# Kernel tuning notes

Hardware: AMD Instinct MI355X
Metric: run time of the kernel (lower is better)

Reference implementation:

```python
import jax, jax.numpy as jnp
import numpy as np

B, T, C = 2, 2048, 2048
H = 16
ROPE_DIM, NOPE_DIM, V_DIM = 64, 64, 128
HEAD_DIM = NOPE_DIM + ROPE_DIM  # 128
Q_RANK, KV_RANK = 1536, 512


def setup_inputs() -> dict:
    key = jax.random.key(0)
    ks = jax.random.split(key, 8)
    std = 0.02
    return {
        "x": jax.random.normal(ks[0], (B, T, C), jnp.float32),
        "cos": jax.random.normal(ks[1], (1, T, 1, ROPE_DIM // 2), jnp.float32),
        "sin": jax.random.normal(ks[2], (1, T, 1, ROPE_DIM // 2), jnp.float32),
        "wq_down": jax.random.normal(ks[3], (Q_RANK, C), jnp.float32) * std,
        "wq_up": jax.random.normal(ks[4], (H * HEAD_DIM, Q_RANK), jnp.float32) * std,
        "wkv_down": jax.random.normal(ks[5], (KV_RANK, C), jnp.float32) * std,
        "wkv_up": jax.random.normal(ks[6], (H * (HEAD_DIM + V_DIM), KV_RANK), jnp.float32) * std,
        "wo": jax.random.normal(ks[7], (C, H * V_DIM), jnp.float32) * std,
    }


def _rope(x, cos, sin):
    # x: [B, T, H, rope_dim]
    d = x.shape[-1] // 2
    x1, x2 = x[..., :d], x[..., d:]
    return jnp.concatenate([x1 * cos + x2 * sin, -x1 * sin + x2 * cos], axis=-1)


def _rms_norm(x):
    eps = jnp.finfo(x.dtype).eps
    return x * jax.lax.rsqrt(jnp.mean(jnp.square(x), axis=-1, keepdims=True) + eps)


def reference(x, cos, sin, wq_down, wq_up, wkv_down, wkv_up, wo):
    # Low-rank q projection
    q = jnp.einsum('btc,rc,dr->btd', x, wq_down, wq_up)
    q = q.reshape(B, T, H, HEAD_DIM)
    q_nope, q_rope = q[..., :NOPE_DIM], q[..., NOPE_DIM:]
    # Low-rank kv projection (naive decompression)
    kv = jnp.einsum('btc,rc,dr->btd', x, wkv_down, wkv_up)
    kv = kv.reshape(B, T, H, HEAD_DIM + V_DIM)
    k_nope = kv[..., :NOPE_DIM]
    k_rope = kv[..., NOPE_DIM:HEAD_DIM]
    v = kv[..., HEAD_DIM:]
    # Partial RoPE on the rope sub-dims only
    q_rope = _rope(q_rope, cos, sin)
    k_rope = _rope(k_rope, cos, sin)
    q = _rms_norm(jnp.concatenate([q_nope, q_rope], axis=-1))
    k = _rms_norm(jnp.concatenate([k_nope, k_rope], axis=-1))
    # Causal SDPA: [B, H, T, T]
    scale = 1.0 / jnp.sqrt(jnp.float32(HEAD_DIM))
    scores = jnp.einsum('bthd,bshd->bhts', q, k) * scale
    causal = jnp.tril(jnp.ones((T, T), dtype=bool))
    scores = jnp.where(causal, scores, jnp.finfo(scores.dtype).min)
    probs = jax.nn.softmax(scores, axis=-1)
    y = jnp.einsum('bhts,bshd->bthd', probs, v).reshape(B, T, H * V_DIM)
    return y @ wo.T
```

## Files before the change

### kernel.cpp

```cpp
#include <hip/hip_runtime.h>
#include <hip/hip_bf16.h>
#include <math.h>
#include <type_traits>

#define AS1 __attribute__((address_space(1)))
#define AS3 __attribute__((address_space(3)))

typedef __bf16  bf16x8 __attribute__((ext_vector_type(8)));
typedef float   f32x4  __attribute__((ext_vector_type(4)));
typedef float   f32x16 __attribute__((ext_vector_type(16)));
typedef __hip_bfloat16 bf16;

#define MFMA16x16x32 __builtin_amdgcn_mfma_f32_16x16x32_bf16
#define MFMA32x32x16 __builtin_amdgcn_mfma_f32_32x32x16_bf16

__device__ __forceinline__ void gload16(const void* g, void* l) {
  __builtin_amdgcn_global_load_lds((const AS1 void*)g, (AS3 void*)l, 16, 0, 0);
}

__device__ __forceinline__ unsigned short bfbits(float v) {
  return __builtin_bit_cast(unsigned short, __float2bfloat16(v));
}

struct CastArgs {
  const float4* src[6];
  ushort4* dst[6];
  unsigned bound[6];
};

__global__ __launch_bounds__(256) void f2bf_multi(CastArgs a) {
  unsigned i = blockIdx.x * 256 + threadIdx.x;
  if (i >= a.bound[5]) return;
  unsigned lo = 0;
  int s = 0;
#pragma unroll
  for (int k = 0; k < 5; k++) {
    if (i >= a.bound[k]) { s = k + 1; lo = a.bound[k]; }
  }
  unsigned idx = i - lo;
  float4 v = a.src[s][idx];
  ushort4 o;
  o.x = bfbits(v.x); o.y = bfbits(v.y); o.z = bfbits(v.z); o.w = bfbits(v.w);
  a.dst[s][idx] = o;
}

template <typename OutT>
__global__ __launch_bounds__(256, 3) void gemm_bt(const bf16* __restrict__ A,
                                                  const bf16* __restrict__ W,
                                                  OutT* __restrict__ Cp,
                                                  int M, int N, int K, int lda) {
  __shared__ __align__(16) bf16 As[128 * 32];
  __shared__ __align__(16) bf16 Ws[128 * 32];
  const int t = threadIdx.x;
  const int w = t >> 6, lane = t & 63;
  const int quad = lane >> 4, l16 = lane & 15;
  const int wr = (w >> 1) * 64, wc = (w & 1) * 64;
  const size_t m0 = (size_t)blockIdx.x * 128;
  const size_t n0 = (size_t)blockIdx.y * 128;
  const int rowS = t >> 2;
  const int kch  = (t & 3) * 8;

  f32x4 acc[4][4];
#pragma unroll
  for (int i = 0; i < 4; i++)
#pragma unroll
    for (int j = 0; j < 4; j++) acc[i][j] = f32x4{0.f, 0.f, 0.f, 0.f};

  for (int k0 = 0; k0 < K; k0 += 32) {
    __syncthreads();
    gload16(A + (m0 + rowS) * (size_t)lda + k0 + kch,      (char*)As + w * 1024);
    gload16(A + (m0 + rowS + 64) * (size_t)lda + k0 + kch, (char*)As + 4096 + w * 1024);
    gload16(W + (n0 + rowS) * (size_t)K + k0 + kch,        (char*)Ws + w * 1024);
    gload16(W + (n0 + rowS + 64) * (size_t)K + k0 + kch,   (char*)Ws + 4096 + w * 1024);
    __syncthreads();

    bf16x8 af[4], bw[4];
#pragma unroll
    for (int i = 0; i < 4; i++)
      af[i] = *(const bf16x8*)(As + (wr + i * 16 + l16) * 32 + quad * 8);
#pragma unroll
    for (int j = 0; j < 4; j++)
      bw[j] = *(const bf16x8*)(Ws + (wc + j * 16 + l16) * 32 + quad * 8);
#pragma unroll
    for (int i = 0; i < 4; i++)
#pragma unroll
      for (int j = 0; j < 4; j++)
        acc[i][j] = MFMA16x16x32(af[i], bw[j], acc[i][j], 0, 0, 0);
  }

#pragma unroll
  for (int i = 0; i < 4; i++)
#pragma unroll
    for (int j = 0; j < 4; j++)
#pragma unroll
      for (int r = 0; r < 4; r++) {
        size_t row = m0 + wr + i * 16 + quad * 4 + r;
        size_t col = n0 + wc + j * 16 + l16;
        float v = acc[i][j][r];
        if constexpr (std::is_same<OutT, float>::value)
          Cp[row * N + col] = v;
        else
          Cp[row * N + col] = __float2bfloat16(v);
      }
}

__global__ __launch_bounds__(256, 3) void gemm_kvup(const bf16* __restrict__ A,
                                                    const bf16* __restrict__ W,
                                                    bf16* __restrict__ kvraw,
                                                    bf16* __restrict__ vT) {
  __shared__ __align__(16) bf16 As[128 * 32];
  __shared__ __align__(16) bf16 Ws[128 * 32];
  const int t = threadIdx.x;
  const int w = t >> 6, lane = t & 63;
  const int quad = lane >> 4, l16 = lane & 15;
  const int wr = (w >> 1) * 64, wc = (w & 1) * 64;
  const size_t m0 = (size_t)blockIdx.x * 128;
  const int n0 = (int)blockIdx.y * 128;
  const int rowS = t >> 2;
  const int kch  = (t & 3) * 8;
  const int K = 512, lda = 2048;

  f32x4 acc[4][4];
#pragma unroll
  for (int i = 0; i < 4; i++)
#pragma unroll
    for (int j = 0; j < 4; j++) acc[i][j] = f32x4{0.f, 0.f, 0.f, 0.f};

  for (int k0 = 0; k0 < K; k0 += 32) {
    __syncthreads();
    gload16(A + (m0 + rowS) * (size_t)lda + k0 + kch,        (char*)As + w * 1024);
    gload16(A + (m0 + rowS + 64) * (size_t)lda + k0 + kch,   (char*)As + 4096 + w * 1024);
    gload16(W + ((size_t)n0 + rowS) * K + k0 + kch,          (char*)Ws + w * 1024);
    gload16(W + ((size_t)n0 + rowS + 64) * K + k0 + kch,     (char*)Ws + 4096 + w * 1024);
    __syncthreads();

    bf16x8 af[4], bw[4];
#pragma unroll
    for (int i = 0; i < 4; i++)
      af[i] = *(const bf16x8*)(As + (wr + i * 16 + l16) * 32 + quad * 8);
#pragma unroll
    for (int j = 0; j < 4; j++)
      bw[j] = *(const bf16x8*)(Ws + (wc + j * 16 + l16) * 32 + quad * 8);
#pragma unroll
    for (int i = 0; i < 4; i++)
#pragma unroll
      for (int j = 0; j < 4; j++)
        acc[i][j] = MFMA16x16x32(af[i], bw[j], acc[i][j], 0, 0, 0);
  }

  if ((n0 & 128) == 0) {
#pragma unroll
    for (int i = 0; i < 4; i++)
#pragma unroll
      for (int j = 0; j < 4; j++)
#pragma unroll
        for (int r = 0; r < 4; r++) {
          size_t row = m0 + wr + i * 16 + quad * 4 + r;
          size_t col = (size_t)n0 + wc + j * 16 + l16;
          kvraw[row * 4096 + col] = __float2bfloat16(acc[i][j][r]);
        }
  } else {
    const int h = n0 >> 8;
#pragma unroll
    for (int i = 0; i < 4; i++) {
      size_t row = m0 + wr + i * 16 + quad * 4;
      int bb = (int)(row >> 11), tloc = (int)(row & 2047);
#pragma unroll
      for (int j = 0; j < 4; j++) {
        int d = wc + j * 16 + l16;
        ushort4 v4;
        v4.x = bfbits(acc[i][j][0]);
        v4.y = bfbits(acc[i][j][1]);
        v4.z = bfbits(acc[i][j][2]);
        v4.w = bfbits(acc[i][j][3]);
        *(ushort4*)(vT + ((size_t)(bb * 16 + h) * 128 + d) * 2048 + tloc) = v4;
      }
    }
  }
}

__global__ __launch_bounds__(256) void rope_rms(const bf16* __restrict__ qraw,
                                                const bf16* __restrict__ kvraw,
                                                const float* __restrict__ cosp,
                                                const float* __restrict__ sinp,
                                                bf16* __restrict__ qn,
                                                bf16* __restrict__ kn) {
  const int bt = blockIdx.x;
  const int w = threadIdx.x >> 6, lane = threadIdx.x & 63;
  const int h = blockIdx.y * 4 + w;
  const int tt = bt & 2047;
  const float c = cosp[tt * 32 + (lane & 31)];
  const float s = sinp[tt * 32 + (lane & 31)];
  const float inv128 = 1.0f / 128.0f;
  const float eps = 1.1920929e-7f;

  {
    const bf16* base = qraw + (size_t)bt * 2048 + h * 128;
    float a = (float)base[lane];
    float o = (float)base[64 + lane];
    float partner = __shfl_xor(o, 32);
    float orope = (lane < 32) ? (o * c + partner * s) : (o * c - partner * s);
    float ss = a * a + orope * orope;
#pragma unroll
    for (int off = 1; off < 64; off <<= 1) ss += __shfl_xor(ss, off);
    float rn = rsqrtf(ss * inv128 + eps);
    bf16* outp = qn + ((size_t)bt * 16 + h) * 128;
    outp[lane] = __float2bfloat16(a * rn);
    outp[64 + lane] = __float2bfloat16(orope * rn);
  }
  {
    const bf16* base = kvraw + (size_t)bt * 4096 + h * 256;
    float a = (float)base[lane];
    float o = (float)base[64 + lane];
    float partner = __shfl_xor(o, 32);
    float orope = (lane < 32) ? (o * c + partner * s) : (o * c - partner * s);
    float ss = a * a + orope * orope;
#pragma unroll
    for (int off = 1; off < 64; off <<= 1) ss += __shfl_xor(ss, off);
    float rn = rsqrtf(ss * inv128 + eps);
    bf16* outp = kn + ((size_t)bt * 16 + h) * 128;
    outp[lane] = __float2bfloat16(a * rn);
    outp[64 + lane] = __float2bfloat16(orope * rn);
  }
}

__global__ __launch_bounds__(128, 2) void attn_kernel(const bf16* __restrict__ qn,
                                                      const bf16* __restrict__ kn,
                                                      const bf16* __restrict__ vT,
                                                      bf16* __restrict__ y) {
  __shared__ __align__(16) bf16 Ks[64 * 128];
  __shared__ __align__(16) bf16 Vs[128 * 64];
  __shared__ __align__(16) bf16 Ps[2][32 * 64];
  const int t = threadIdx.x, w = t >> 6, lane = t & 63;
  const int l32 = lane & 31, hl = lane >> 5;
  const int b = blockIdx.x >> 4, h = blockIdx.x & 15;
  const int yy = (int)blockIdx.y;
  const int y0 = yy & 7, k4 = yy >> 3;
  int xb;
  if (k4 == 0) xb = 31 - y0;
  else if (k4 == 1) xb = y0;
  else if (k4 == 2) xb = 23 - y0;
  else xb = 8 + y0;
  const int q0 = xb * 64;
  const int T_ = 2048, H_ = 16;

  bf16x8 qf[8];
  {
    const bf16* qbase = qn + ((size_t)(b * T_ + q0 + w * 32 + l32) * H_ + h) * 128;
#pragma unroll
    for (int ki = 0; ki < 8; ki++)
      qf[ki] = *(const bf16x8*)(qbase + ki * 16 + hl * 8);
  }

  f32x16 yacc[4];
#pragma unroll
  for (int db = 0; db < 4; db++)
#pragma unroll
    for (int i = 0; i < 16; i++) yacc[db][i] = 0.f;
  float lrow[16];
#pragma unroll
  for (int r = 0; r < 16; r++) lrow[r] = 0.f;
  const float K1 = 0.08838834764831845f * 1.4426950408889634f;
  const float K2 = -12.0f * 1.4426950408889634f;
  const int ntiles = xb + 1;

  for (int it = 0; it < ntiles; ++it) {
    const int s0 = it * 64;
    __syncthreads();
#pragma unroll
    for (int is = 0; is < 8; ++is) {
      int i = is * 2 + w;
      int srow = i * 4 + (lane >> 4);
      int cg = (lane & 15) ^ (srow & 7);
      gload16(kn + ((size_t)(b * T_ + s0 + srow) * H_ + h) * 128 + cg * 8,
              (char*)Ks + i * 1024);
    }
#pragma unroll
    for (int is = 0; is < 8; ++is) {
      int i = is * 2 + w;
      int drow = i * 8 + (lane >> 3);
      int cg = (lane & 7) ^ (drow & 7);
      gload16(vT + ((size_t)(b * H_ + h) * 128 + drow) * T_ + s0 + cg * 8,
              (char*)Vs + i * 1024);
    }
    __syncthreads();

    f32x16 sacc[2];
#pragma unroll
    for (int cb = 0; cb < 2; cb++)
#pragma unroll
      for (int i = 0; i < 16; i++) sacc[cb][i] = 0.f;
#pragma unroll
    for (int cb = 0; cb < 2; ++cb) {
      const int s = cb * 32 + l32;
#pragma unroll
      for (int ki = 0; ki < 8; ++ki) {
        int pos = (ki * 2 + hl) ^ (s & 7);
        bf16x8 kf = *(const bf16x8*)(Ks + s * 128 + pos * 8);
        sacc[cb] = MFMA32x32x16(qf[ki], kf, sacc[cb], 0, 0, 0);
      }
    }

    const bool diag = (it == xb);
#pragma unroll
    for (int cb = 0; cb < 2; ++cb) {
      const int sidx = cb * 32 + l32;
      const int sg = s0 + sidx;
#pragma unroll
      for (int r = 0; r < 16; ++r) {
        const int row = (r & 3) + 8 * (r >> 2) + 4 * hl;
        float e;
        if (diag && (sg > q0 + w * 32 + row))
          e = 0.0f;
        else
          e = exp2f(fmaf(sacc[cb][r], K1, K2));
        lrow[r] += e;
        Ps[w][row * 64 + (((sidx >> 3) ^ (row & 7)) << 3) + (sidx & 7)] =
            __float2bfloat16(e);
      }
    }
    __asm__ volatile("s_waitcnt lgkmcnt(0)" ::: "memory");

#pragma unroll
    for (int ki = 0; ki < 4; ++ki) {
      int ppos = (ki * 2 + hl) ^ (l32 & 7);
      bf16x8 pf = *(const bf16x8*)(&Ps[w][l32 * 64 + ppos * 8]);
#pragma unroll
      for (int db = 0; db < 4; ++db) {
        int d = db * 32 + l32;
        int vpos = (ki * 2 + hl) ^ (d & 7);
        bf16x8 vf = *(const bf16x8*)(Vs + d * 64 + vpos * 8);
        yacc[db] = MFMA32x32x16(pf, vf, yacc[db], 0, 0, 0);
      }
    }
  }

#pragma unroll
  for (int r = 0; r < 16; r++) {
#pragma unroll
    for (int off = 1; off < 32; off <<= 1) lrow[r] += __shfl_xor(lrow[r], off);
  }
#pragma unroll
  for (int r = 0; r < 16; r++) {
    const int row = (r & 3) + 8 * (r >> 2) + 4 * hl;
    float inv = 1.0f / lrow[r];
    size_t qrow = (size_t)(b * T_ + q0 + w * 32 + row);
    bf16* outp = y + qrow * 2048 + h * 128;
#pragma unroll
    for (int db = 0; db < 4; db++)
      outp[db * 32 + l32] = __float2bfloat16(yacc[db][r] * inv);
  }
}

extern "C" void kernel_launch(void* const* d_in, const int* in_sizes, int n_in,
                              void* d_out, int out_size, void* d_ws, size_t ws_size,
                              hipStream_t stream) {
  (void)in_sizes; (void)n_in; (void)out_size; (void)ws_size;
  const float* x    = (const float*)d_in[0];
  const float* cosp = (const float*)d_in[1];
  const float* sinp = (const float*)d_in[2];
  const float* wqd  = (const float*)d_in[3];
  const float* wqu  = (const float*)d_in[4];
  const float* wkvd = (const float*)d_in[5];
  const float* wkvu = (const float*)d_in[6];
  const float* wo   = (const float*)d_in[7];
  float* out = (float*)d_out;

  char* ws = (char*)d_ws;
  size_t off = 0;
  auto alloc = [&](size_t elems) { bf16* p = (bf16*)(ws + off); off += elems * 2; return p; };
  bf16* xb      = alloc((size_t)4096 * 2048);
  bf16* wqdB    = alloc((size_t)1536 * 2048);
  bf16* wkvdB   = alloc((size_t)512 * 2048);
  bf16* wquB    = alloc((size_t)2048 * 1536);
  bf16* wkvuB   = alloc((size_t)4096 * 512);
  bf16* woB     = alloc((size_t)2048 * 2048);
  bf16* qkvdown = alloc((size_t)4096 * 2048);
  bf16* qraw    = alloc((size_t)4096 * 2048);
  bf16* kvraw   = alloc((size_t)4096 * 4096);
  bf16* qnb     = alloc((size_t)4096 * 16 * 128);
  bf16* knb     = alloc((size_t)4096 * 16 * 128);
  bf16* vTb     = alloc((size_t)2 * 16 * 128 * 2048);
  bf16* yb      = alloc((size_t)4096 * 2048);

  CastArgs ca;
  const float* srcs[6] = {x, wqd, wkvd, wqu, wkvu, wo};
  bf16* dsts[6]        = {xb, wqdB, wkvdB, wquB, wkvuB, woB};
  size_t cnts[6] = {(size_t)4096 * 2048, (size_t)1536 * 2048, (size_t)512 * 2048,
                    (size_t)2048 * 1536, (size_t)4096 * 512,  (size_t)2048 * 2048};
  unsigned cum = 0;
  for (int i = 0; i < 6; i++) {
    ca.src[i] = (const float4*)srcs[i];
    ca.dst[i] = (ushort4*)dsts[i];
    cum += (unsigned)(cnts[i] / 4);
    ca.bound[i] = cum;
  }
  f2bf_multi<<<dim3((cum + 255) / 256), 256, 0, stream>>>(ca);

  gemm_bt<bf16><<<dim3(32, 16), 256, 0, stream>>>(xb, wqdB, qkvdown, 4096, 2048, 2048, 2048);
  gemm_bt<bf16><<<dim3(32, 16), 256, 0, stream>>>(qkvdown, wquB, qraw, 4096, 2048, 1536, 2048);
  gemm_kvup<<<dim3(32, 32), 256, 0, stream>>>(qkvdown + 1536, wkvuB, kvraw, vTb);
  rope_rms<<<dim3(4096, 4), 256, 0, stream>>>(qraw, kvraw, cosp, sinp, qnb, knb);
  attn_kernel<<<dim3(32, 32), 128, 0, stream>>>(qnb, knb, vTb, yb);
  gemm_bt<float><<<dim3(32, 16), 256, 0, stream>>>(yb, woB, out, 4096, 2048, 2048, 2048);
}
```

Measured before the change: 393.8 us.

## Split attention block into four 16-row waves using 16x16x32 MFMA

The attention kernel now runs each 64-query block with four wavefronts of 16 rows each, instead of two wavefronts of 32 rows. It switches from 32x32x16 to 16x16x32 MFMA and reorganises the Q, score, P and output fragment layouts to match. K/V tile loads are now spread over four waves, and each thread holds fewer registers. The goal is more waves per CU, better latency hiding and less load per wave, at the cost of a lower MFMA tile size and more LDS traffic per FLOP, since V fragments are reread per 16-row wave.

```diff
diff --git a/kernel.cpp b/kernel.cpp
--- a/kernel.cpp
+++ b/kernel.cpp
@@ -8,11 +8,9 @@
 
 typedef __bf16  bf16x8 __attribute__((ext_vector_type(8)));
 typedef float   f32x4  __attribute__((ext_vector_type(4)));
-typedef float   f32x16 __attribute__((ext_vector_type(16)));
 typedef __hip_bfloat16 bf16;
 
 #define MFMA16x16x32 __builtin_amdgcn_mfma_f32_16x16x32_bf16
-#define MFMA32x32x16 __builtin_amdgcn_mfma_f32_32x32x16_bf16
 
 __device__ __forceinline__ void gload16(const void* g, void* l) {
   __builtin_amdgcn_global_load_lds((const AS1 void*)g, (AS3 void*)l, 16, 0, 0);
@@ -224,15 +222,15 @@
   }
 }
 
-__global__ __launch_bounds__(128, 2) void attn_kernel(const bf16* __restrict__ qn,
+__global__ __launch_bounds__(256, 4) void attn_kernel(const bf16* __restrict__ qn,
                                                       const bf16* __restrict__ kn,
                                                       const bf16* __restrict__ vT,
                                                       bf16* __restrict__ y) {
   __shared__ __align__(16) bf16 Ks[64 * 128];
   __shared__ __align__(16) bf16 Vs[128 * 64];
-  __shared__ __align__(16) bf16 Ps[2][32 * 64];
+  __shared__ __align__(16) bf16 Ps[4][16 * 64];
   const int t = threadIdx.x, w = t >> 6, lane = t & 63;
-  const int l32 = lane & 31, hl = lane >> 5;
+  const int quad = lane >> 4, l16 = lane & 15;
   const int b = blockIdx.x >> 4, h = blockIdx.x & 15;
   const int yy = (int)blockIdx.y;
   const int y0 = yy & 7, k4 = yy >> 3;
@@ -244,22 +242,16 @@
   const int q0 = xb * 64;
   const int T_ = 2048, H_ = 16;
 
-  bf16x8 qf[8];
+  bf16x8 qf[4];
   {
-    const bf16* qbase = qn + ((size_t)(b * T_ + q0 + w * 32 + l32) * H_ + h) * 128;
-#pragma unroll
-    for (int ki = 0; ki < 8; ki++)
-      qf[ki] = *(const bf16x8*)(qbase + ki * 16 + hl * 8);
-  }
-
-  f32x16 yacc[4];
-#pragma unroll
-  for (int db = 0; db < 4; db++)
-#pragma unroll
-    for (int i = 0; i < 16; i++) yacc[db][i] = 0.f;
-  float lrow[16];
-#pragma unroll
-  for (int r = 0; r < 16; r++) lrow[r] = 0.f;
+    const bf16* qbase = qn + ((size_t)(b * T_ + q0 + w * 16 + l16) * H_ + h) * 128;
+#pragma unroll
+    for (int ks = 0; ks < 4; ks++) qf[ks] = *(const bf16x8*)(qbase + ks * 32 + quad * 8);
+  }
+  f32x4 yacc[8];
+#pragma unroll
+  for (int i = 0; i < 8; i++) yacc[i] = f32x4{0.f, 0.f, 0.f, 0.f};
+  float lrow[4] = {0.f, 0.f, 0.f, 0.f};
   const float K1 = 0.08838834764831845f * 1.4426950408889634f;
   const float K2 = -12.0f * 1.4426950408889634f;
   const int ntiles = xb + 1;
@@ -268,87 +260,89 @@
     const int s0 = it * 64;
     __syncthreads();
 #pragma unroll
-    for (int is = 0; is < 8; ++is) {
-      int i = is * 2 + w;
-      int srow = i * 4 + (lane >> 4);
-      int cg = (lane & 15) ^ (srow & 7);
+    for (int is = 0; is < 4; ++is) {
+      int srow = is * 16 + w * 4 + quad;
+      int cg = l16 ^ (srow & 7);
       gload16(kn + ((size_t)(b * T_ + s0 + srow) * H_ + h) * 128 + cg * 8,
-              (char*)Ks + i * 1024);
+              (char*)Ks + is * 4096 + w * 1024);
     }
 #pragma unroll
-    for (int is = 0; is < 8; ++is) {
-      int i = is * 2 + w;
-      int drow = i * 8 + (lane >> 3);
+    for (int is = 0; is < 4; ++is) {
+      int drow = is * 32 + w * 8 + (lane >> 3);
       int cg = (lane & 7) ^ (drow & 7);
       gload16(vT + ((size_t)(b * H_ + h) * 128 + drow) * T_ + s0 + cg * 8,
-              (char*)Vs + i * 1024);
+              (char*)Vs + is * 4096 + w * 1024);
     }
     __syncthreads();
 
-    f32x16 sacc[2];
-#pragma unroll
-    for (int cb = 0; cb < 2; cb++)
-#pragma unroll
-      for (int i = 0; i < 16; i++) sacc[cb][i] = 0.f;
-#pragma unroll
-    for (int cb = 0; cb < 2; ++cb) {
-      const int s = cb * 32 + l32;
-#pragma unroll
-      for (int ki = 0; ki < 8; ++ki) {
-        int pos = (ki * 2 + hl) ^ (s & 7);
-        bf16x8 kf = *(const bf16x8*)(Ks + s * 128 + pos * 8);
-        sacc[cb] = MFMA32x32x16(qf[ki], kf, sacc[cb], 0, 0, 0);
+    f32x4 sacc[4];
+#pragma unroll
+    for (int cg = 0; cg < 4; cg++) sacc[cg] = f32x4{0.f, 0.f, 0.f, 0.f};
+#pragma unroll
+    for (int cg = 0; cg < 4; ++cg) {
+      const int srow = cg * 16 + l16;
+#pragma unroll
+      for (int ks = 0; ks < 4; ++ks) {
+        int pos = (ks * 4 + quad) ^ (srow & 7);
+        bf16x8 kf = *(const bf16x8*)(Ks + srow * 128 + pos * 8);
+        sacc[cg] = MFMA16x16x32(qf[ks], kf, sacc[cg], 0, 0, 0);
       }
     }
 
     const bool diag = (it == xb);
-#pragma unroll
-    for (int cb = 0; cb < 2; ++cb) {
-      const int sidx = cb * 32 + l32;
-      const int sg = s0 + sidx;
-#pragma unroll
-      for (int r = 0; r < 16; ++r) {
-        const int row = (r & 3) + 8 * (r >> 2) + 4 * hl;
+    float p[4][4];
+#pragma unroll
+    for (int cg = 0; cg < 4; ++cg)
+#pragma unroll
+      for (int r = 0; r < 4; ++r) {
         float e;
-        if (diag && (sg > q0 + w * 32 + row))
+        if (diag && (cg * 16 + l16 > w * 16 + quad * 4 + r))
           e = 0.0f;
         else
-          e = exp2f(fmaf(sacc[cb][r], K1, K2));
+          e = exp2f(fmaf(sacc[cg][r], K1, K2));
+        p[cg][r] = e;
         lrow[r] += e;
-        Ps[w][row * 64 + (((sidx >> 3) ^ (row & 7)) << 3) + (sidx & 7)] =
-            __float2bfloat16(e);
+      }
+
+#pragma unroll
+    for (int cg = 0; cg < 4; cg++)
+#pragma unroll
+      for (int r = 0; r < 4; r++) {
+        const int row = quad * 4 + r;
+        const int col = cg * 16 + l16;
+        Ps[w][row * 64 + (((col >> 3) ^ (row & 7)) << 3) + (col & 7)] =
+            __float2bfloat16(p[cg][r]);
+      }
+    __asm__ volatile("s_waitcnt lgkmcnt(0)" ::: "memory");
+
+    bf16x8 pf[2];
+#pragma unroll
+    for (int k2 = 0; k2 < 2; k2++)
+      pf[k2] = *(const bf16x8*)(&Ps[w][l16 * 64 + (((k2 * 4 + quad) ^ (l16 & 7)) << 3)]);
+#pragma unroll
+    for (int dg = 0; dg < 8; dg++) {
+      const int drow = dg * 16 + l16;
+#pragma unroll
+      for (int k2 = 0; k2 < 2; k2++) {
+        int pos = (k2 * 4 + quad) ^ (drow & 7);
+        bf16x8 vf = *(const bf16x8*)(Vs + drow * 64 + pos * 8);
+        yacc[dg] = MFMA16x16x32(pf[k2], vf, yacc[dg], 0, 0, 0);
       }
     }
-    __asm__ volatile("s_waitcnt lgkmcnt(0)" ::: "memory");
-
-#pragma unroll
-    for (int ki = 0; ki < 4; ++ki) {
-      int ppos = (ki * 2 + hl) ^ (l32 & 7);
-      bf16x8 pf = *(const bf16x8*)(&Ps[w][l32 * 64 + ppos * 8]);
-#pragma unroll
-      for (int db = 0; db < 4; ++db) {
-        int d = db * 32 + l32;
-        int vpos = (ki * 2 + hl) ^ (d & 7);
-        bf16x8 vf = *(const bf16x8*)(Vs + d * 64 + vpos * 8);
-        yacc[db] = MFMA32x32x16(pf, vf, yacc[db], 0, 0, 0);
-      }
-    }
-  }
-
-#pragma unroll
-  for (int r = 0; r < 16; r++) {
-#pragma unroll
-    for (int off = 1; off < 32; off <<= 1) lrow[r] += __shfl_xor(lrow[r], off);
-  }
-#pragma unroll
-  for (int r = 0; r < 16; r++) {
-    const int row = (r & 3) + 8 * (r >> 2) + 4 * hl;
+  }
+
+#pragma unroll
+  for (int off = 1; off < 16; off <<= 1)
+#pragma unroll
+    for (int r = 0; r < 4; r++) lrow[r] += __shfl_xor(lrow[r], off);
+#pragma unroll
+  for (int r = 0; r < 4; r++) {
     float inv = 1.0f / lrow[r];
-    size_t qrow = (size_t)(b * T_ + q0 + w * 32 + row);
+    size_t qrow = (size_t)(b * T_ + q0 + w * 16 + quad * 4 + r);
     bf16* outp = y + qrow * 2048 + h * 128;
 #pragma unroll
-    for (int db = 0; db < 4; db++)
-      outp[db * 32 + l32] = __float2bfloat16(yacc[db][r] * inv);
+    for (int dg = 0; dg < 8; dg++)
+      outp[dg * 16 + l16] = __float2bfloat16(yacc[dg][r] * inv);
   }
 }
 
@@ -401,6 +395,6 @@
   gemm_bt<bf16><<<dim3(32, 16), 256, 0, stream>>>(qkvdown, wquB, qraw, 4096, 2048, 1536, 2048);
   gemm_kvup<<<dim3(32, 32), 256, 0, stream>>>(qkvdown + 1536, wkvuB, kvraw, vTb);
   rope_rms<<<dim3(4096, 4), 256, 0, stream>>>(qraw, kvraw, cosp, sinp, qnb, knb);
-  attn_kernel<<<dim3(32, 32), 128, 0, stream>>>(qnb, knb, vTb, yb);
+  attn_kernel<<<dim3(32, 32), 256, 0, stream>>>(qnb, knb, vTb, yb);
   gemm_bt<float><<<dim3(32, 16), 256, 0, stream>>>(yb, woB, out, 4096, 2048, 2048, 2048);
 }
```

Result: faster. 375.8 us (-4.6%).

## Double-buffer K/V tiles and widen attention blocks to 128 query rows

Applied to the files above, without the earlier changes.

The attention kernel now runs 4 waves per block covering 128 query rows, so each K/V tile loaded into LDS is shared by twice as many queries. The grid is halved and reshuffled to pair heavy and light causal blocks. K and V tiles are double-buffered: the next tile is issued with async global-to-LDS loads right after the barrier, so the load overlaps the current tile's MFMA work and one barrier per iteration is removed. In exchange, LDS use per block grows to about 80 KB, which may limit how many blocks fit on a CU, and there are fewer blocks in total.

```diff
diff --git a/kernel.cpp b/kernel.cpp
--- a/kernel.cpp
+++ b/kernel.cpp
@@ -224,24 +224,20 @@
   }
 }
 
-__global__ __launch_bounds__(128, 2) void attn_kernel(const bf16* __restrict__ qn,
+__global__ __launch_bounds__(256, 2) void attn_kernel(const bf16* __restrict__ qn,
                                                       const bf16* __restrict__ kn,
                                                       const bf16* __restrict__ vT,
                                                       bf16* __restrict__ y) {
-  __shared__ __align__(16) bf16 Ks[64 * 128];
-  __shared__ __align__(16) bf16 Vs[128 * 64];
-  __shared__ __align__(16) bf16 Ps[2][32 * 64];
+  __shared__ __align__(16) bf16 Ks[2][64 * 128];
+  __shared__ __align__(16) bf16 Vs[2][128 * 64];
+  __shared__ __align__(16) bf16 Ps[4][32 * 64];
   const int t = threadIdx.x, w = t >> 6, lane = t & 63;
   const int l32 = lane & 31, hl = lane >> 5;
   const int b = blockIdx.x >> 4, h = blockIdx.x & 15;
   const int yy = (int)blockIdx.y;
-  const int y0 = yy & 7, k4 = yy >> 3;
-  int xb;
-  if (k4 == 0) xb = 31 - y0;
-  else if (k4 == 1) xb = y0;
-  else if (k4 == 2) xb = 23 - y0;
-  else xb = 8 + y0;
-  const int q0 = xb * 64;
+  const int y0 = yy & 7;
+  const int xb = (yy < 8) ? (15 - y0) : y0;
+  const int q0 = xb * 128;
   const int T_ = 2048, H_ = 16;
 
   bf16x8 qf[8];
@@ -262,28 +258,33 @@
   for (int r = 0; r < 16; r++) lrow[r] = 0.f;
   const float K1 = 0.08838834764831845f * 1.4426950408889634f;
   const float K2 = -12.0f * 1.4426950408889634f;
-  const int ntiles = xb + 1;
+  const int ntiles = 2 * xb + 2;
+
+  auto stage = [&](int it, int bsel) {
+    const int s0 = it * 64;
+#pragma unroll
+    for (int is = 0; is < 4; ++is) {
+      int srow = is * 16 + w * 4 + (lane >> 4);
+      int cg = (lane & 15) ^ (srow & 7);
+      gload16(kn + ((size_t)(b * T_ + s0 + srow) * H_ + h) * 128 + cg * 8,
+              (char*)Ks[bsel] + is * 4096 + w * 1024);
+    }
+#pragma unroll
+    for (int is = 0; is < 4; ++is) {
+      int drow = is * 32 + w * 8 + (lane >> 3);
+      int cg = (lane & 7) ^ (drow & 7);
+      gload16(vT + ((size_t)(b * H_ + h) * 128 + drow) * T_ + s0 + cg * 8,
+              (char*)Vs[bsel] + is * 4096 + w * 1024);
+    }
+  };
+
+  stage(0, 0);
 
   for (int it = 0; it < ntiles; ++it) {
+    const int bsel = it & 1;
     const int s0 = it * 64;
     __syncthreads();
-#pragma unroll
-    for (int is = 0; is < 8; ++is) {
-      int i = is * 2 + w;
-      int srow = i * 4 + (lane >> 4);
-      int cg = (lane & 15) ^ (srow & 7);
-      gload16(kn + ((size_t)(b * T_ + s0 + srow) * H_ + h) * 128 + cg * 8,
-              (char*)Ks + i * 1024);
-    }
-#pragma unroll
-    for (int is = 0; is < 8; ++is) {
-      int i = is * 2 + w;
-      int drow = i * 8 + (lane >> 3);
-      int cg = (lane & 7) ^ (drow & 7);
-      gload16(vT + ((size_t)(b * H_ + h) * 128 + drow) * T_ + s0 + cg * 8,
-              (char*)Vs + i * 1024);
-    }
-    __syncthreads();
+    if (it + 1 < ntiles) stage(it + 1, bsel ^ 1);
 
     f32x16 sacc[2];
 #pragma unroll
@@ -296,12 +297,12 @@
 #pragma unroll
       for (int ki = 0; ki < 8; ++ki) {
         int pos = (ki * 2 + hl) ^ (s & 7);
-        bf16x8 kf = *(const bf16x8*)(Ks + s * 128 + pos * 8);
+        bf16x8 kf = *(const bf16x8*)(Ks[bsel] + s * 128 + pos * 8);
         sacc[cb] = MFMA32x32x16(qf[ki], kf, sacc[cb], 0, 0, 0);
       }
     }
 
-    const bool diag = (it == xb);
+    const bool diag = (it >= ntiles - 2);
 #pragma unroll
     for (int cb = 0; cb < 2; ++cb) {
       const int sidx = cb * 32 + l32;
@@ -329,7 +330,7 @@
       for (int db = 0; db < 4; ++db) {
         int d = db * 32 + l32;
         int vpos = (ki * 2 + hl) ^ (d & 7);
-        bf16x8 vf = *(const bf16x8*)(Vs + d * 64 + vpos * 8);
+        bf16x8 vf = *(const bf16x8*)(Vs[bsel] + d * 64 + vpos * 8);
         yacc[db] = MFMA32x32x16(pf, vf, yacc[db], 0, 0, 0);
       }
     }
@@ -401,6 +402,6 @@
   gemm_bt<bf16><<<dim3(32, 16), 256, 0, stream>>>(qkvdown, wquB, qraw, 4096, 2048, 1536, 2048);
   gemm_kvup<<<dim3(32, 32), 256, 0, stream>>>(qkvdown + 1536, wkvuB, kvraw, vTb);
   rope_rms<<<dim3(4096, 4), 256, 0, stream>>>(qraw, kvraw, cosp, sinp, qnb, knb);
-  attn_kernel<<<dim3(32, 32), 128, 0, stream>>>(qnb, knb, vTb, yb);
+  attn_kernel<<<dim3(32, 16), 256, 0, stream>>>(qnb, knb, vTb, yb);
   gemm_bt<float><<<dim3(32, 16), 256, 0, stream>>>(yb, woB, out, 4096, 2048, 2048, 2048);
 }
```

After: 384.2 us. -2.4%, faster.
